# Kernel optimization log

Measured on AMD Instinct MI355X. Metric: run time of the kernel, lower is better.

## Reference

```python
import jax, jax.numpy as jnp
import numpy as np

N_NODES = 10000
N_REL = 200
DIM = 128          # rank * 2
REL_DIM = 128
VIS_DIM = 512
TXT_DIM = 768
N_EDGES = 320000


def _glorot(key, shape):
    fan_in, fan_out = shape[1], shape[0]
    lim = (6.0 / (fan_in + fan_out)) ** 0.5
    return jax.random.uniform(key, shape, jnp.float32, -lim, lim)


def setup_inputs() -> dict:
    key = jax.random.key(0)
    ks = jax.random.split(key, 24)
    inp = {}
    inp['x'] = jax.random.randint(ks[0], (1024, 3), 0, N_NODES)
    inp['edge_index'] = jax.random.randint(ks[1], (2, N_EDGES), 0, N_NODES)
    inp['edge_type'] = jax.random.randint(ks[2], (N_EDGES,), 0, N_REL)
    inp['visual'] = jax.random.normal(ks[3], (N_NODES, VIS_DIM), jnp.float32)
    inp['textual'] = jax.random.normal(ks[4], (N_NODES, TXT_DIM), jnp.float32)
    # embeddings (scaled by 0.001 as in torch init)
    inp['structural_emb'] = jax.random.normal(ks[5], (N_NODES, DIM), jnp.float32) * 0.001
    inp['relation_emb'] = jax.random.normal(ks[6], (N_REL, REL_DIM), jnp.float32) * 0.001
    # three KBGAT convs: w1 [out, 2*in+rel], b1 [out], w2 [1, out]
    cat = 2 * DIM + REL_DIM
    for i, tag in enumerate(['s', 'v', 't']):
        inp[f'W1_{tag}'] = _glorot(ks[7 + 3 * i], (DIM, cat))
        inp[f'b1_{tag}'] = jnp.zeros((DIM,), jnp.float32)
        inp[f'w2_{tag}'] = _glorot(ks[8 + 3 * i], (1, DIM))
    # modality projections
    inp['Wv'] = _glorot(ks[16], (DIM, VIS_DIM))
    inp['bv'] = jnp.zeros((DIM,), jnp.float32)
    inp['Wt'] = _glorot(ks[17], (DIM, TXT_DIM))
    inp['bt'] = jnp.zeros((DIM,), jnp.float32)
    inp['alpha'] = jnp.float32(0.1)
    inp['gamma'] = jnp.float32(0.8)
    return inp


def kbgat_conv(feat, rel_emb, src, dst, edge_type, W1, b1, w2):
    # gather per-edge embeddings: x_i = target, x_j = source (PyG default flow)
    triple = jnp.concatenate([feat[dst], feat[src], rel_emb[edge_type]], axis=1)  # [E, 2*D+R]
    c = triple @ W1.T + b1                                   # [E, D]
    b = jax.nn.leaky_relu(c @ w2[0])                         # [E]
    # segment softmax over destination nodes
    m = jax.ops.segment_max(b, dst, num_segments=N_NODES)
    e = jnp.exp(b - m[dst])
    z = jax.ops.segment_sum(e, dst, num_segments=N_NODES)
    attn = e / z[dst]                                        # [E]
    agg = jax.ops.segment_sum(c * attn[:, None], dst, num_segments=N_NODES)  # [N, D]
    return jax.nn.leaky_relu(agg)


def reference(x, edge_index, edge_type, visual, textual, structural_emb, relation_emb,
              W1_s, b1_s, w2_s, W1_v, b1_v, w2_v, W1_t, b1_t, w2_t,
              Wv, bv, Wt, bt, alpha, gamma):
    src, dst = edge_index[0], edge_index[1]
    h_s = kbgat_conv(structural_emb, relation_emb, src, dst, edge_type, W1_s, b1_s, w2_s)
    vf = visual @ Wv.T + bv
    h_v = kbgat_conv(vf, relation_emb, src, dst, edge_type, W1_v, b1_v, w2_v)
    tf = textual @ Wt.T + bt
    h_t = kbgat_conv(tf, relation_emb, src, dst, edge_type, W1_t, b1_t, w2_t)
    return (1.0 - alpha - gamma) * h_s + alpha * h_v + gamma * h_t
```

## Files before the change

### kernel.cpp

```cpp
#include <hip/hip_runtime.h>
#include <hip/hip_bf16.h>

typedef unsigned short u16;
typedef unsigned int u32;
typedef __bf16 bf16x8 __attribute__((ext_vector_type(8)));
typedef float f32x4 __attribute__((ext_vector_type(4)));

#define DIM 128

__device__ __forceinline__ u16 f2bf_rne(float x) {
  u32 u = __float_as_uint(x);
  return (u16)((u + 0x7fffu + ((u >> 16) & 1u)) >> 16);
}
__device__ __forceinline__ u32 packbf2(float x, float y) {
  return (u32)f2bf_rne(x) | ((u32)f2bf_rne(y) << 16);
}
__device__ __forceinline__ float lrelu(float x) { return x > 0.f ? x : 0.01f * x; }
__device__ __forceinline__ int iclamp(int v, int hi) { return v < 0 ? 0 : (v >= hi ? hi - 1 : v); }
__device__ __forceinline__ float sane(float x) { return (x == x) ? x : 0.f; }

__device__ __forceinline__ float wred_max(float v) {
  #pragma unroll
  for (int o = 32; o > 0; o >>= 1) v = fmaxf(v, __shfl_xor(v, o, 64));
  return v;
}
__device__ __forceinline__ float wred_sum(float v) {
  #pragma unroll
  for (int o = 32; o > 0; o >>= 1) v += __shfl_xor(v, o, 64);
  return v;
}

__global__ void hist_k(const int* __restrict__ dst, int* __restrict__ cnt, int E, int N) {
  int e = blockIdx.x * blockDim.x + threadIdx.x;
  if (e < E) {
    int d = dst[e];
    if (d >= 0 && d < N) atomicAdd(&cnt[d], 1);
  }
}

__global__ __launch_bounds__(1024) void scan_k(const int* __restrict__ cnt,
                                               int* __restrict__ offs, int N) {
  __shared__ int sums[1024];
  int t = threadIdx.x;
  int chunk = (N + 1023) >> 10;
  int base = t * chunk;
  int s = 0;
  for (int i = 0; i < chunk; ++i) { int idx = base + i; if (idx < N) s += cnt[idx]; }
  sums[t] = s;
  __syncthreads();
  for (int off = 1; off < 1024; off <<= 1) {
    int v = (t >= off) ? sums[t - off] : 0;
    __syncthreads();
    sums[t] += v;
    __syncthreads();
  }
  int prefix = (t > 0) ? sums[t - 1] : 0;
  for (int i = 0; i < chunk; ++i) {
    int idx = base + i;
    if (idx < N) { offs[idx] = prefix; prefix += cnt[idx]; }
  }
  if (t == 1023) offs[N] = sums[1023];
}

__global__ void scatter_k(const int* __restrict__ dst, const int* __restrict__ src,
                          const int* __restrict__ etyp,
                          const int* __restrict__ offs,
                          int* __restrict__ cursor, u32* __restrict__ sortedST,
                          int E, int N, int NR) {
  int e = blockIdx.x * blockDim.x + threadIdx.x;
  if (e < E) {
    int d = dst[e];
    if (d >= 0 && d < N) {
      int pos = offs[d] + atomicAdd(&cursor[d], 1);
      if (pos >= 0 && pos < E) {
        u32 s = (u32)iclamp(src[e], N);
        u32 t = (u32)iclamp(etyp[e], NR);
        sortedST[pos] = (t << 16) | s;
      }
    }
  }
}

struct PrepArgs {
  const float* W1[3]; const float* Wmod[3]; int K[3]; int isCopy[3];
  u16* Wc[3];
};
struct PrArgs {
  const float* rel; const float* W1[3]; const float* b1[3];
  const float* bmod[3]; const float* w2[3];
  u16* PrAll; float* qr[3]; int NR;
};
struct GArgs {
  const float* A[3]; const u16* B[3]; const float* w2[3];
  u16* PdAll; u16* PsAll; float* qd[3]; float* qs[3];
  int M; int K[3];
};
struct AgArgs {
  const u32* sortedST; const int* offs;
  const float* qd[3]; const float* qs[3]; const float* qr[3];
  const u16* PdAll; const u16* PsAll; const u16* PrAll;
  const float* alphaP; const float* gammaP;
  float* outp; int N; int NR; int E;
};

__global__ void prep_wc_all(PrepArgs a) {
  int m = blockIdx.z;
  int K = a.K[m];
  int k = blockIdx.x * blockDim.x + threadIdx.x;
  int o = blockIdx.y;
  if (k >= K) return;
  int half = (o >= 128) ? 128 : 0;
  int oo = o & 127;
  const float* W1 = a.W1[m];
  float acc;
  if (a.isCopy[m]) {
    acc = W1[oo * 384 + half + k];
  } else {
    const float* Wm = a.Wmod[m];
    acc = 0.f;
    for (int i = 0; i < 128; ++i)
      acc += W1[oo * 384 + half + i] * Wm[i * K + k];
  }
  a.Wc[m][((size_t)(k >> 5) * 256 + o) * 32 + (k & 31)] = f2bf_rne(acc);
}

__global__ __launch_bounds__(128) void prep_pr_all(PrArgs a) {
  __shared__ float red[128];
  int m = blockIdx.z;
  int r = blockIdx.x;
  if (r >= a.NR) return;
  int o = threadIdx.x;
  const float* W1 = a.W1[m];
  float acc = a.b1[m][o];
  for (int i = 0; i < 128; ++i)
    acc += W1[o * 384 + 256 + i] * a.rel[r * 128 + i];
  const float* bmod = a.bmod[m];
  if (bmod != nullptr) {
    for (int i = 0; i < 128; ++i)
      acc += (W1[o * 384 + i] + W1[o * 384 + 128 + i]) * bmod[i];
  }
  a.PrAll[(size_t)r * 384 + m * 128 + o] = f2bf_rne(acc);
  red[o] = acc * a.w2[m][o];
  __syncthreads();
  for (int s = 64; s > 0; s >>= 1) {
    if (o < s) red[o] += red[o + s];
    __syncthreads();
  }
  if (o == 0) a.qr[m][r] = sane(red[0]);
}

__global__ __launch_bounds__(256) void gemm_fused(GArgs g) {
  __shared__ u16 Als[8 * 64 * 32];
  __shared__ float qpart[4][64];
  int m = blockIdx.y;
  int M = g.M, K = g.K[m];
  int nt = K >> 5;
  const u16* Bpk = g.B[m];
  const float* w2 = g.w2[m];
  int tid = threadIdx.x;
  int lane = tid & 63, wv = tid >> 6;
  int quad = lane >> 4, l16 = lane & 15;
  int row0 = blockIdx.x * 64;

  int srow = tid >> 2;
  int kseg = (tid & 3) * 64;
  int grow = row0 + srow;
  if (grow >= M) grow = M - 1;
  const float* Ag = g.A[m] + (size_t)grow * K;

  const u16* Bpg = Bpk + (size_t)(wv * 64 + l16) * 32 + quad * 8;

  f32x4 acc[4][4];
  #pragma unroll
  for (int rg = 0; rg < 4; ++rg)
    #pragma unroll
    for (int t = 0; t < 4; ++t) acc[rg][t] = (f32x4){0.f, 0.f, 0.f, 0.f};

  int nchunk = (nt + 7) >> 3;
  for (int c = 0; c < nchunk; ++c) {
    int kbase = c << 8;
    __syncthreads();
    #pragma unroll
    for (int i = 0; i < 16; ++i) {
      int kl = kseg + i * 4;
      int kg = kbase + kl;
      if (kg < K) {
        float4 v = *reinterpret_cast<const float4*>(Ag + kg);
        u32* d = reinterpret_cast<u32*>(&Als[((kl >> 5) * 64 + srow) * 32 + (kl & 31)]);
        d[0] = packbf2(v.x, v.y);
        d[1] = packbf2(v.z, v.w);
      }
    }
    __syncthreads();
    int kbR = nt - (c << 3);
    if (kbR > 8) kbR = 8;
    for (int kbl = 0; kbl < kbR; ++kbl) {
      const u16* bp = Bpg + (size_t)((c << 3) + kbl) * 8192;
      bf16x8 b0 = *reinterpret_cast<const bf16x8*>(bp);
      bf16x8 b1 = *reinterpret_cast<const bf16x8*>(bp + 512);
      bf16x8 b2 = *reinterpret_cast<const bf16x8*>(bp + 1024);
      bf16x8 b3 = *reinterpret_cast<const bf16x8*>(bp + 1536);
      #pragma unroll
      for (int rg = 0; rg < 4; ++rg) {
        bf16x8 a = *reinterpret_cast<const bf16x8*>(
            &Als[(kbl * 64 + rg * 16 + l16) * 32 + quad * 8]);
        acc[rg][0] = __builtin_amdgcn_mfma_f32_16x16x32_bf16(a, b0, acc[rg][0], 0, 0, 0);
        acc[rg][1] = __builtin_amdgcn_mfma_f32_16x16x32_bf16(a, b1, acc[rg][1], 0, 0, 0);
        acc[rg][2] = __builtin_amdgcn_mfma_f32_16x16x32_bf16(a, b2, acc[rg][2], 0, 0, 0);
        acc[rg][3] = __builtin_amdgcn_mfma_f32_16x16x32_bf16(a, b3, acc[rg][3], 0, 0, 0);
      }
    }
  }

  u16* PdAll = g.PdAll;
  u16* PsAll = g.PsAll;
  float w2c[4];
  #pragma unroll
  for (int t = 0; t < 4; ++t) w2c[t] = w2[(wv & 1) * 64 + t * 16 + l16];

  #pragma unroll
  for (int rg = 0; rg < 4; ++rg) {
    float part[4];
    #pragma unroll
    for (int r = 0; r < 4; ++r) {
      int rr = row0 + rg * 16 + quad * 4 + r;
      bool ok = rr < M;
      float qp = 0.f;
      #pragma unroll
      for (int t = 0; t < 4; ++t) {
        int cc = (wv & 1) * 64 + t * 16 + l16;
        if (ok) {
          if (wv < 2) PdAll[(size_t)rr * 384 + m * 128 + cc] = f2bf_rne(acc[rg][t][r]);
          else        PsAll[(size_t)rr * 384 + m * 128 + cc] = f2bf_rne(acc[rg][t][r]);
        }
        qp += acc[rg][t][r] * w2c[t];
      }
      #pragma unroll
      for (int mk = 1; mk < 16; mk <<= 1) qp += __shfl_xor(qp, mk, 64);
      part[r] = qp;
    }
    if (l16 == 0) {
      #pragma unroll
      for (int r = 0; r < 4; ++r) qpart[wv][rg * 16 + quad * 4 + r] = part[r];
    }
  }
  __syncthreads();
  if (tid < 128) {
    int row = tid & 63;
    int half = tid >> 6;
    int rr = row0 + row;
    if (rr < M) {
      if (half == 0) g.qd[m][rr] = sane(qpart[0][row] + qpart[1][row]);
      else           g.qs[m][rr] = sane(qpart[2][row] + qpart[3][row]);
    }
  }
}

__global__ __launch_bounds__(256) void aggregate_all(AgArgs a) {
  int n = blockIdx.x * 4 + (threadIdx.x >> 6);
  if (n >= a.N) return;
  int lane = threadIdx.x & 63;
  int E = a.E;
  int eb = a.offs[n], ee = a.offs[n + 1];
  if (eb < 0) eb = 0;
  if (eb > E) eb = E;
  if (ee < eb) ee = eb;
  if (ee > E) ee = E;
  int En = ee - eb;

  float al = a.alphaP[0];
  if (!(al > 0.f && al < 1.f)) al = 0.1f;
  float ga = a.gammaP[0];
  if (!(ga > 0.f && ga < 1.f)) ga = 0.8f;
  float coef[3] = {1.f - al - ga, al, ga};

  float qdn[3];
  #pragma unroll
  for (int m = 0; m < 3; ++m) qdn[m] = sane(a.qd[m][n]);

  const u16* PsAll = a.PsAll;
  const u16* PrAll = a.PrAll;
  int dlo = 2 * lane;

  float rm[3] = {-1e30f, -1e30f, -1e30f};
  float z[3] = {0.f, 0.f, 0.f};
  float a0[3] = {0.f, 0.f, 0.f};
  float a1[3] = {0.f, 0.f, 0.f};
  for (int c0 = 0; c0 < En; c0 += 64) {
    int cn = min(64, En - c0);
    u32 stp = 0;
    float bm[3] = {-1e30f, -1e30f, -1e30f};
    if (lane < cn) {
      stp = a.sortedST[eb + c0 + lane];
      int s = (int)(stp & 0xffffu);
      int t = (int)(stp >> 16);
      #pragma unroll
      for (int m = 0; m < 3; ++m)
        bm[m] = lrelu(qdn[m] + a.qs[m][s] + a.qr[m][t]);
    }
    float wr[3];
    #pragma unroll
    for (int m = 0; m < 3; ++m) {
      float cm = wred_max(bm[m]);
      float nm = fmaxf(rm[m], cm);
      float sc = __expf(fmaxf(rm[m] - nm, -80.f));
      z[m] *= sc; a0[m] *= sc; a1[m] *= sc;
      rm[m] = nm;
      wr[m] = (lane < cn) ? __expf(fmaxf(bm[m] - nm, -80.f)) : 0.f;
      z[m] += wr[m];
    }

    int cnR = (cn + 3) & ~3;
    for (int j = 0; j < cnR; j += 4) {
      u32 stj[4];
      float wj[4][3];
      #pragma unroll
      for (int u = 0; u < 4; ++u) {
        stj[u] = __shfl(stp, j + u, 64);
        wj[u][0] = __shfl(wr[0], j + u, 64);
        wj[u][1] = __shfl(wr[1], j + u, 64);
        wj[u][2] = __shfl(wr[2], j + u, 64);
      }
      u32 pu[4][3], ru[4][3];
      #pragma unroll
      for (int u = 0; u < 4; ++u) {
        const u16* ps = PsAll + (size_t)(stj[u] & 0xffffu) * 384 + dlo;
        const u16* pr = PrAll + (size_t)(stj[u] >> 16) * 384 + dlo;
        #pragma unroll
        for (int m = 0; m < 3; ++m) {
          pu[u][m] = *reinterpret_cast<const u32*>(ps + m * 128);
          ru[u][m] = *reinterpret_cast<const u32*>(pr + m * 128);
        }
      }
      #pragma unroll
      for (int u = 0; u < 4; ++u) {
        #pragma unroll
        for (int m = 0; m < 3; ++m) {
          float ps0 = __uint_as_float(pu[u][m] << 16);
          float ps1 = __uint_as_float(pu[u][m] & 0xffff0000u);
          float pr0 = __uint_as_float(ru[u][m] << 16);
          float pr1 = __uint_as_float(ru[u][m] & 0xffff0000u);
          a0[m] = fmaf(wj[u][m], ps0 + pr0, a0[m]);
          a1[m] = fmaf(wj[u][m], ps1 + pr1, a1[m]);
        }
      }
    }
  }
  #pragma unroll
  for (int m = 0; m < 3; ++m) z[m] = wred_sum(z[m]);

  float o0 = 0.f, o1 = 0.f;
  const u16* pd = a.PdAll + (size_t)n * 384 + dlo;
  #pragma unroll
  for (int m = 0; m < 3; ++m) {
    float h0 = 0.f, h1 = 0.f;
    if (En > 0 && z[m] > 0.f) {
      float rz = 1.f / z[m];
      u32 du = *reinterpret_cast<const u32*>(pd + m * 128);
      float pd0 = __uint_as_float(du << 16), pd1 = __uint_as_float(du & 0xffff0000u);
      h0 = lrelu(pd0 + a0[m] * rz);
      h1 = lrelu(pd1 + a1[m] * rz);
    }
    o0 = fmaf(coef[m], h0, o0);
    o1 = fmaf(coef[m], h1, o1);
  }
  float* op = a.outp + (size_t)n * 128 + dlo;
  op[0] = sane(o0);
  op[1] = sane(o1);
}

extern "C" void kernel_launch(void* const* d_in, const int* in_sizes, int n_in,
                              void* d_out, int out_size, void* d_ws, size_t ws_size,
                              hipStream_t stream) {
  const int* ei        = (const int*)d_in[1];
  const int* et        = (const int*)d_in[2];
  const float* visual  = (const float*)d_in[3];
  const float* textual = (const float*)d_in[4];
  const float* semb    = (const float*)d_in[5];
  const float* relemb  = (const float*)d_in[6];
  const float* W1s = (const float*)d_in[7];
  const float* b1s = (const float*)d_in[8];
  const float* w2s = (const float*)d_in[9];
  const float* W1v = (const float*)d_in[10];
  const float* b1v = (const float*)d_in[11];
  const float* w2v = (const float*)d_in[12];
  const float* W1t = (const float*)d_in[13];
  const float* b1t = (const float*)d_in[14];
  const float* w2t = (const float*)d_in[15];
  const float* Wv  = (const float*)d_in[16];
  const float* bv  = (const float*)d_in[17];
  const float* Wt  = (const float*)d_in[18];
  const float* bt  = (const float*)d_in[19];
  const float* alphaP = (const float*)d_in[20];
  const float* gammaP = (const float*)d_in[21];
  float* outp = (float*)d_out;

  const int E   = in_sizes[2];
  const int N   = in_sizes[5] / DIM;
  const int NR  = in_sizes[6] / DIM;
  const int VIS = in_sizes[3] / N;
  const int TXT = in_sizes[4] / N;
  const int KMAX = (TXT > VIS) ? TXT : VIS;
  int Ks[3] = {DIM, VIS, TXT};
  const int NT64 = (N + 63) / 64;

  const float* W1a[3]   = {W1s, W1v, W1t};
  const float* b1a[3]   = {b1s, b1v, b1t};
  const float* w2a[3]   = {w2s, w2v, w2t};
  const float* Wmoda[3] = {nullptr, Wv, Wt};
  const float* bmoda[3] = {nullptr, bv, bt};
  const float* Amoda[3] = {semb, visual, textual};

  const int* esrc = ei;
  const int* edst = ei + E;
  int egrid = (E + 255) / 256;

  size_t off = 0;
  auto take = [&](size_t bytes) -> size_t {
    size_t o = off;
    off = (off + bytes + 255) & ~(size_t)255;
    return o;
  };
  size_t o_cnt  = take((size_t)2 * N * 4);
  size_t o_offs = take((size_t)(N + 1) * 4);
  size_t o_st   = take((size_t)E * 4);
  size_t meta_end = off;
  size_t o_qdm[3], o_qsm[3], o_qrm[3], o_Wcm[3];
  for (int m = 0; m < 3; ++m) {
    o_qdm[m] = take((size_t)N * 4);
    o_qsm[m] = take((size_t)N * 4);
    o_qrm[m] = take((size_t)NR * 4);
    o_Wcm[m] = take((size_t)256 * Ks[m] * 2);
  }
  size_t o_PrAll = take((size_t)NR * 384 * 2);
  size_t o_PdAll = take((size_t)N * 384 * 2);
  size_t o_PsAll = take((size_t)N * 384 * 2);
  size_t need = off;

  if (ws_size < need) {
    hipMemsetAsync(d_out, 0, (size_t)out_size * 4, stream);
    return;
  }

  char* w = (char*)d_ws;
  int* counts = (int*)(w + o_cnt);
  int* cursor = counts + N;
  int* offs   = (int*)(w + o_offs);
  u32* sortedST = (u32*)(w + o_st);

  hipMemsetAsync(w, 0, meta_end, stream);
  hist_k<<<egrid, 256, 0, stream>>>(edst, counts, E, N);
  scan_k<<<1, 1024, 0, stream>>>(counts, offs, N);
  scatter_k<<<egrid, 256, 0, stream>>>(edst, esrc, et, offs, cursor, sortedST, E, N, NR);

  PrepArgs pa;
  PrArgs ra;
  GArgs ga;
  AgArgs aa;
  ra.rel = relemb; ra.NR = NR;
  ra.PrAll = (u16*)(w + o_PrAll);
  ga.M = N;
  ga.PdAll = (u16*)(w + o_PdAll);
  ga.PsAll = (u16*)(w + o_PsAll);
  for (int m = 0; m < 3; ++m) {
    pa.W1[m] = W1a[m]; pa.Wmod[m] = Wmoda[m]; pa.K[m] = Ks[m];
    pa.isCopy[m] = (m == 0);
    pa.Wc[m] = (u16*)(w + o_Wcm[m]);
    ra.W1[m] = W1a[m]; ra.b1[m] = b1a[m]; ra.bmod[m] = bmoda[m]; ra.w2[m] = w2a[m];
    ra.qr[m] = (float*)(w + o_qrm[m]);
    ga.A[m] = Amoda[m]; ga.B[m] = (const u16*)(w + o_Wcm[m]); ga.w2[m] = w2a[m];
    ga.qd[m] = (float*)(w + o_qdm[m]); ga.qs[m] = (float*)(w + o_qsm[m]);
    ga.K[m] = Ks[m];
    aa.qd[m] = (const float*)(w + o_qdm[m]);
    aa.qs[m] = (const float*)(w + o_qsm[m]);
    aa.qr[m] = (const float*)(w + o_qrm[m]);
  }
  aa.PdAll = (const u16*)(w + o_PdAll);
  aa.PsAll = (const u16*)(w + o_PsAll);
  aa.PrAll = (const u16*)(w + o_PrAll);
  aa.sortedST = sortedST; aa.offs = offs;
  aa.alphaP = alphaP; aa.gammaP = gammaP;
  aa.outp = outp; aa.N = N; aa.NR = NR; aa.E = E;

  prep_wc_all<<<dim3((KMAX + 255) / 256, 256, 3), 256, 0, stream>>>(pa);
  prep_pr_all<<<dim3(NR, 1, 3), 128, 0, stream>>>(ra);
  gemm_fused<<<dim3(NT64, 3), 256, 0, stream>>>(ga);
  aggregate_all<<<(N + 3) / 4, 256, 0, stream>>>(aa);
}
```

Measured before the change: 277.6 us.

## Shrink GEMM row tile to 32, swizzle LDS, order heavy modality blocks first

The fused projection GEMM now uses 32-row tiles instead of 64, launched as a flat 1D grid in which textual (K=768) blocks are scheduled first, then visual, then structural. The LDS A-tile gets an XOR swizzle to reduce bank conflicts on MFMA operand reads, and launch bounds request 4 blocks per CU. The metadata memset is narrowed to just the counts/cursor arrays. More, smaller blocks raise occupancy and balance the load, but each block reloads B from global memory per row, doubling B traffic.

```diff
diff --git a/kernel.cpp b/kernel.cpp
--- a/kernel.cpp
+++ b/kernel.cpp
@@ -93,7 +93,7 @@
 struct GArgs {
   const float* A[3]; const u16* B[3]; const float* w2[3];
   u16* PdAll; u16* PsAll; float* qd[3]; float* qs[3];
-  int M; int K[3];
+  int M; int K[3]; int tilesPerM;
 };
 struct AgArgs {
   const u32* sortedST; const int* offs;
@@ -149,10 +149,16 @@
   if (o == 0) a.qr[m][r] = sane(red[0]);
 }
 
-__global__ __launch_bounds__(256) void gemm_fused(GArgs g) {
-  __shared__ u16 Als[8 * 64 * 32];
-  __shared__ float qpart[4][64];
-  int m = blockIdx.y;
+__global__ __launch_bounds__(256, 4) void gemm_fused(GArgs g) {
+  __shared__ __align__(16) u16 Als[8 * 32 * 32];
+  __shared__ float qpart[4][32];
+  int fb = blockIdx.x;
+  int tpm = g.tilesPerM;
+  int m, tile;
+  if (fb < tpm)            { m = 2; tile = fb; }
+  else if (fb < 2 * tpm)   { m = 1; tile = fb - tpm; }
+  else                     { m = 0; tile = fb - 2 * tpm; }
+
   int M = g.M, K = g.K[m];
   int nt = K >> 5;
   const u16* Bpk = g.B[m];
@@ -160,19 +166,22 @@
   int tid = threadIdx.x;
   int lane = tid & 63, wv = tid >> 6;
   int quad = lane >> 4, l16 = lane & 15;
-  int row0 = blockIdx.x * 64;
-
-  int srow = tid >> 2;
-  int kseg = (tid & 3) * 64;
+  int row0 = tile * 32;
+
+  int srow = tid >> 3;
+  int tk4 = (tid & 7) * 4;
+  int srsw = srow & 3;
+  int wg = tk4 >> 3;
+  int wrem = tk4 & 7;
   int grow = row0 + srow;
   if (grow >= M) grow = M - 1;
   const float* Ag = g.A[m] + (size_t)grow * K;
 
   const u16* Bpg = Bpk + (size_t)(wv * 64 + l16) * 32 + quad * 8;
 
-  f32x4 acc[4][4];
-  #pragma unroll
-  for (int rg = 0; rg < 4; ++rg)
+  f32x4 acc[2][4];
+  #pragma unroll
+  for (int rg = 0; rg < 2; ++rg)
     #pragma unroll
     for (int t = 0; t < 4; ++t) acc[rg][t] = (f32x4){0.f, 0.f, 0.f, 0.f};
 
@@ -181,12 +190,14 @@
     int kbase = c << 8;
     __syncthreads();
     #pragma unroll
-    for (int i = 0; i < 16; ++i) {
-      int kl = kseg + i * 4;
+    for (int i = 0; i < 8; ++i) {
+      int kl = tk4 + i * 32;
       int kg = kbase + kl;
       if (kg < K) {
         float4 v = *reinterpret_cast<const float4*>(Ag + kg);
-        u32* d = reinterpret_cast<u32*>(&Als[((kl >> 5) * 64 + srow) * 32 + (kl & 31)]);
+        int gidx = wg ^ srsw ^ (i & 3);
+        u32* d = reinterpret_cast<u32*>(
+            &Als[((i * 32 + srow) * 32) + (gidx << 3) + wrem]);
         d[0] = packbf2(v.x, v.y);
         d[1] = packbf2(v.z, v.w);
       }
@@ -200,10 +211,11 @@
       bf16x8 b1 = *reinterpret_cast<const bf16x8*>(bp + 512);
       bf16x8 b2 = *reinterpret_cast<const bf16x8*>(bp + 1024);
       bf16x8 b3 = *reinterpret_cast<const bf16x8*>(bp + 1536);
-      #pragma unroll
-      for (int rg = 0; rg < 4; ++rg) {
+      int gsw = (quad ^ (l16 & 3) ^ (kbl & 3)) << 3;
+      #pragma unroll
+      for (int rg = 0; rg < 2; ++rg) {
         bf16x8 a = *reinterpret_cast<const bf16x8*>(
-            &Als[(kbl * 64 + rg * 16 + l16) * 32 + quad * 8]);
+            &Als[(kbl * 32 + rg * 16 + l16) * 32 + gsw]);
         acc[rg][0] = __builtin_amdgcn_mfma_f32_16x16x32_bf16(a, b0, acc[rg][0], 0, 0, 0);
         acc[rg][1] = __builtin_amdgcn_mfma_f32_16x16x32_bf16(a, b1, acc[rg][1], 0, 0, 0);
         acc[rg][2] = __builtin_amdgcn_mfma_f32_16x16x32_bf16(a, b2, acc[rg][2], 0, 0, 0);
@@ -219,7 +231,7 @@
   for (int t = 0; t < 4; ++t) w2c[t] = w2[(wv & 1) * 64 + t * 16 + l16];
 
   #pragma unroll
-  for (int rg = 0; rg < 4; ++rg) {
+  for (int rg = 0; rg < 2; ++rg) {
     float part[4];
     #pragma unroll
     for (int r = 0; r < 4; ++r) {
@@ -245,9 +257,9 @@
     }
   }
   __syncthreads();
-  if (tid < 128) {
-    int row = tid & 63;
-    int half = tid >> 6;
+  if (tid < 64) {
+    int row = tid & 31;
+    int half = tid >> 5;
     int rr = row0 + row;
     if (rr < M) {
       if (half == 0) g.qd[m][rr] = sane(qpart[0][row] + qpart[1][row]);
@@ -402,7 +414,7 @@
   const int TXT = in_sizes[4] / N;
   const int KMAX = (TXT > VIS) ? TXT : VIS;
   int Ks[3] = {DIM, VIS, TXT};
-  const int NT64 = (N + 63) / 64;
+  const int TPM = (N + 31) / 32;
 
   const float* W1a[3]   = {W1s, W1v, W1t};
   const float* b1a[3]   = {b1s, b1v, b1t};
@@ -424,7 +436,6 @@
   size_t o_cnt  = take((size_t)2 * N * 4);
   size_t o_offs = take((size_t)(N + 1) * 4);
   size_t o_st   = take((size_t)E * 4);
-  size_t meta_end = off;
   size_t o_qdm[3], o_qsm[3], o_qrm[3], o_Wcm[3];
   for (int m = 0; m < 3; ++m) {
     o_qdm[m] = take((size_t)N * 4);
@@ -448,7 +459,7 @@
   int* offs   = (int*)(w + o_offs);
   u32* sortedST = (u32*)(w + o_st);
 
-  hipMemsetAsync(w, 0, meta_end, stream);
+  hipMemsetAsync(w, 0, (size_t)2 * N * 4, stream);
   hist_k<<<egrid, 256, 0, stream>>>(edst, counts, E, N);
   scan_k<<<1, 1024, 0, stream>>>(counts, offs, N);
   scatter_k<<<egrid, 256, 0, stream>>>(edst, esrc, et, offs, cursor, sortedST, E, N, NR);
@@ -460,6 +471,7 @@
   ra.rel = relemb; ra.NR = NR;
   ra.PrAll = (u16*)(w + o_PrAll);
   ga.M = N;
+  ga.tilesPerM = TPM;
   ga.PdAll = (u16*)(w + o_PdAll);
   ga.PsAll = (u16*)(w + o_PsAll);
   for (int m = 0; m < 3; ++m) {
@@ -484,6 +496,6 @@
 
   prep_wc_all<<<dim3((KMAX + 255) / 256, 256, 3), 256, 0, stream>>>(pa);
   prep_pr_all<<<dim3(NR, 1, 3), 128, 0, stream>>>(ra);
-  gemm_fused<<<dim3(NT64, 3), 256, 0, stream>>>(ga);
+  gemm_fused<<<dim3(3 * TPM), 256, 0, stream>>>(ga);
   aggregate_all<<<(N + 3) / 4, 256, 0, stream>>>(aa);
 }
```

Measured after the change: 277.4 us. No clear change (-0.1%).
